# Optimization experiments

Measured on AMD Instinct MI355X. Metric: run time of the kernel, lower is better.

## Reference

```python
import jax, jax.numpy as jnp
import numpy as np

EMBED_DIM = 256
NUM_HEADS = 8
HEAD_DIM = EMBED_DIM // NUM_HEADS
SCALE = HEAD_DIM ** (-0.5)
L, B = 2048, 2


def setup_inputs() -> dict:
    key = jax.random.key(0)
    ks = jax.random.split(key, 12)
    s = EMBED_DIM ** (-0.5)
    return {
        "query": jax.random.normal(ks[0], (L, B, EMBED_DIM), jnp.float32),
        "key_": jax.random.normal(ks[1], (L, B, EMBED_DIM), jnp.float32),
        "value": jax.random.normal(ks[2], (L, B, EMBED_DIM), jnp.float32),
        "Wq": jax.random.normal(ks[3], (EMBED_DIM, EMBED_DIM), jnp.float32) * s,
        "bq": jnp.zeros((EMBED_DIM,), jnp.float32),
        "Wk": jax.random.normal(ks[4], (EMBED_DIM, EMBED_DIM), jnp.float32) * s,
        "bk": jnp.zeros((EMBED_DIM,), jnp.float32),
        "Wv": jax.random.normal(ks[5], (EMBED_DIM, EMBED_DIM), jnp.float32) * s,
        "bv": jnp.zeros((EMBED_DIM,), jnp.float32),
        "Wp": jax.random.normal(ks[6], (EMBED_DIM, EMBED_DIM), jnp.float32) * s,
        "bp": jnp.zeros((EMBED_DIM,), jnp.float32),
    }


def reference(query, key_, value, Wq, bq, Wk, bk, Wv, bv, Wp, bp):
    # Inputs are seq-first: [L, B, E]. Dropout treated as eval (identity).
    Lq, Bq, E = query.shape
    q = (query @ Wq + bq).reshape(Lq, Bq, NUM_HEADS, HEAD_DIM)
    k = (key_ @ Wk + bk).reshape(key_.shape[0], Bq, NUM_HEADS, HEAD_DIM)
    v = (value @ Wv + bv).reshape(value.shape[0], Bq, NUM_HEADS, HEAD_DIM)
    # scores: [B, H, Lq, Lk]
    attn = jnp.einsum('qbhd,kbhd->bhqk', q, k) * SCALE
    attn = jax.nn.softmax(attn, axis=-1)
    out = jnp.einsum('bhqk,kbhd->qbhd', attn, v).reshape(Lq, Bq, E)
    return out @ Wp + bp
```

## Files before the change

kernel.cpp:

```cpp
#include <hip/hip_runtime.h>
#include <math.h>

#define L_SEQ 2048
#define BATCH 2
#define EMB   256
#define NH    8
#define HD    32
#define NROW  (L_SEQ * BATCH)
#define SCALE 0.17677669529663687f
#define LOG2E 1.4426950408889634f

typedef __attribute__((ext_vector_type(8))) short          short8;
typedef __attribute__((ext_vector_type(8))) unsigned short ushort8v;
typedef __attribute__((ext_vector_type(4))) unsigned short ushort4v;
typedef __attribute__((ext_vector_type(4))) float          floatx4;

__device__ __forceinline__ unsigned short f2b(float x) {
    unsigned int u = __float_as_uint(x);
    unsigned int r = u + 0x7FFFu + ((u >> 16) & 1u);
    return (unsigned short)(r >> 16);
}

__device__ __forceinline__ unsigned int pack2bf(float lo, float hi) {
    unsigned int ulo = __float_as_uint(lo);
    unsigned int uhi = __float_as_uint(hi);
    ulo += 0x7FFFu + ((ulo >> 16) & 1u);
    uhi += 0x7FFFu + ((uhi >> 16) & 1u);
    return __builtin_amdgcn_perm(uhi, ulo, 0x07060302);
}

__device__ __forceinline__ float b2f(unsigned short u) {
    return __uint_as_float(((unsigned int)u) << 16);
}

__device__ __forceinline__ float hw_exp2(float x) {
    return __builtin_amdgcn_exp2f(x);
}

__global__ __launch_bounds__(256) void wtrans_kernel(const float* __restrict__ Wq,
                                                     const float* __restrict__ Wk,
                                                     const float* __restrict__ Wv,
                                                     const float* __restrict__ Wp,
                                                     unsigned short* __restrict__ out) {
    __shared__ unsigned short T[64][65];
    const int wsel = blockIdx.z;
    const float* W = (wsel == 0) ? Wq : (wsel == 1) ? Wk : (wsel == 2) ? Wv : Wp;
    const float scale = (wsel == 0) ? (SCALE * LOG2E) : 1.0f;
    unsigned short* dst = out + (size_t)wsel * EMB * EMB;
    const int k0 = blockIdx.x * 64, n0 = blockIdx.y * 64;
    const int tid = threadIdx.x;

    #pragma unroll
    for (int i = 0; i < 4; ++i) {
        int idx = tid + 256 * i;
        int r = idx >> 4, c4 = (idx & 15) * 4;
        float4 f = *(const float4*)&W[(size_t)(k0 + r) * EMB + n0 + c4];
        T[r][c4 + 0] = f2b(f.x * scale);
        T[r][c4 + 1] = f2b(f.y * scale);
        T[r][c4 + 2] = f2b(f.z * scale);
        T[r][c4 + 3] = f2b(f.w * scale);
    }
    __syncthreads();
    #pragma unroll
    for (int i = 0; i < 4; ++i) {
        int idx = tid + 256 * i;
        int rn = idx >> 4, ck = (idx & 15) * 4;
        ushort4v p;
        #pragma unroll
        for (int j = 0; j < 4; ++j) p[j] = T[ck + j][rn];
        *(ushort4v*)&dst[(size_t)(n0 + rn) * EMB + k0 + ck] = p;
    }
}

__global__ __launch_bounds__(256) void qkv_proj(const float* __restrict__ Xq,
                                                const float* __restrict__ Xk,
                                                const float* __restrict__ Xv,
                                                const unsigned short* __restrict__ Wt,
                                                const float* __restrict__ bq,
                                                const float* __restrict__ bk,
                                                const float* __restrict__ bv,
                                                unsigned short* __restrict__ outq,
                                                unsigned short* __restrict__ outk,
                                                unsigned short* __restrict__ outvt) {
    __shared__ unsigned short Xs[64][136];
    __shared__ unsigned short Ws[64][136];
    const int z = blockIdx.z;
    const float* X    = (z == 0) ? Xq : (z == 1) ? Xk : Xv;
    const float* bias = (z == 0) ? bq : (z == 1) ? bk : bv;
    const float bscale = (z == 0) ? (SCALE * LOG2E) : 1.0f;
    const unsigned short* W = Wt + (size_t)z * EMB * EMB;

    const int row0 = blockIdx.x * 64;
    const int col0 = blockIdx.y * 64;
    const int tid  = threadIdx.x;
    const int w    = tid >> 6;
    const int lane = tid & 63;
    const int l16  = lane & 15;
    const int quad = lane >> 4;
    const floatx4 zero4 = {0.f, 0.f, 0.f, 0.f};

    floatx4 acc[4] = {zero4, zero4, zero4, zero4};

    #pragma unroll
    for (int kh = 0; kh < 2; ++kh) {
        if (kh) __syncthreads();
        #pragma unroll
        for (int i = 0; i < 4; ++i) {
            int idx = tid + 256 * i;
            int r = idx >> 4, c8 = (idx & 15) * 8;
            const float4* xp = (const float4*)&X[(size_t)(row0 + r) * EMB + kh * 128 + c8];
            float4 f0 = xp[0], f1 = xp[1];
            uint4 pk;
            pk.x = pack2bf(f0.x, f0.y); pk.y = pack2bf(f0.z, f0.w);
            pk.z = pack2bf(f1.x, f1.y); pk.w = pack2bf(f1.z, f1.w);
            *(uint4*)&Xs[r][c8] = pk;
            *(ushort8v*)&Ws[r][c8] =
                *(const ushort8v*)&W[(size_t)(col0 + r) * EMB + kh * 128 + c8];
        }
        __syncthreads();

        #pragma unroll
        for (int k = 0; k < 128; k += 32) {
            short8 a = *(const short8*)&Xs[w * 16 + l16][k + quad * 8];
            #pragma unroll
            for (int g = 0; g < 4; ++g) {
                short8 bf = *(const short8*)&Ws[g * 16 + l16][k + quad * 8];
                acc[g] = __builtin_amdgcn_mfma_f32_16x16x32_bf16(a, bf, acc[g], 0, 0, 0);
            }
        }
    }

    if (z == 2) {
        __syncthreads();
        #pragma unroll
        for (int g = 0; g < 4; ++g) {
            int n = g * 16 + l16;
            float bb = bias[col0 + n] * bscale;
            #pragma unroll
            for (int r = 0; r < 4; ++r)
                Xs[w * 16 + quad * 4 + r][n] = f2b(acc[g][r] + bb);
        }
        __syncthreads();
        #pragma unroll
        for (int i = 0; i < 2; ++i) {
            int idx = tid + 256 * i;
            int n = idx >> 3, sub = idx & 7;
            int bb2 = sub >> 2, lq = sub & 3;
            ushort8v p;
            #pragma unroll
            for (int j = 0; j < 8; ++j) p[j] = Xs[(lq * 8 + j) * 2 + bb2][n];
            int h = (col0 + n) >> 5, d = (col0 + n) & 31;
            size_t base = ((size_t)(bb2 * NH + h) * HD + d) * L_SEQ + (row0 >> 1) + lq * 8;
            *(ushort8v*)&outvt[base] = p;
        }
    } else {
        unsigned short* outp = z ? outk : outq;
        #pragma unroll
        for (int g = 0; g < 4; ++g) {
            int c = col0 + g * 16 + l16;
            float bb = bias[c] * bscale;
            #pragma unroll
            for (int r = 0; r < 4; ++r) {
                int rg = row0 + w * 16 + quad * 4 + r;
                int b = rg & 1, ll = rg >> 1;
                int h = c >> 5, d = c & 31;
                outp[(((size_t)(b * NH + h) * L_SEQ) + ll) * HD + d] = f2b(acc[g][r] + bb);
            }
        }
    }
}

__global__ __launch_bounds__(256) void attn_kernel(const unsigned short* __restrict__ Q,
                                                   const unsigned short* __restrict__ K,
                                                   const unsigned short* __restrict__ Vt,
                                                   unsigned short* __restrict__ Opart,
                                                   float* __restrict__ lpart) {
    __shared__ unsigned short Vs[2][32][136];
    __shared__ unsigned short Ps[4][16][136];

    const int tid  = threadIdx.x;
    const int w    = tid >> 6;
    const int lane = tid & 63;
    const int l16  = lane & 15;
    const int quad = lane >> 4;

    const int l0   = blockIdx.x * 64;
    const int h    = blockIdx.y;
    const int b    = blockIdx.z & 1;
    const int half = blockIdx.z >> 1;
    const int koff = half * (L_SEQ / 2);
    const size_t bh = (size_t)(b * NH + h);

    const unsigned short* Qg  = Q  + (bh * L_SEQ) * HD;
    const unsigned short* Kg  = K  + (bh * L_SEQ + koff) * HD;
    const unsigned short* Vtg = Vt + (bh * HD) * L_SEQ + koff;

    short8 qfrag = *(const short8*)&Qg[(size_t)(l0 + w * 16 + l16) * HD + quad * 8];

    float lacc = 0.0f;
    const floatx4 zero4 = {0.f, 0.f, 0.f, 0.f};
    floatx4 o0 = zero4, o1 = zero4;

    const int vd = tid >> 3;
    const int vj = (tid & 7) * 8;

    short8 kf[8];
    #pragma unroll
    for (int g = 0; g < 8; ++g)
        kf[g] = *(const short8*)&Kg[(size_t)(g * 16 + l16) * HD + quad * 8];

    *(ushort8v*)&Vs[0][vd][vj]      = *(const ushort8v*)&Vtg[(size_t)vd * L_SEQ + vj];
    *(ushort8v*)&Vs[0][vd][64 + vj] = *(const ushort8v*)&Vtg[(size_t)vd * L_SEQ + 64 + vj];

    const int NT = (L_SEQ / 2) / 128;
    for (int kt = 0; kt < NT; ++kt) {
        __syncthreads();

        floatx4 s[8];
        #pragma unroll
        for (int g = 0; g < 8; ++g)
            s[g] = __builtin_amdgcn_mfma_f32_16x16x32_bf16(kf[g], qfrag, zero4, 0, 0, 0);

        ushort8v vn0, vn1;
        if (kt + 1 < NT) {
            #pragma unroll
            for (int g = 0; g < 8; ++g)
                kf[g] = *(const short8*)
                    &Kg[(size_t)((kt + 1) * 128 + g * 16 + l16) * HD + quad * 8];
            vn0 = *(const ushort8v*)&Vtg[(size_t)vd * L_SEQ + (kt + 1) * 128 + vj];
            vn1 = *(const ushort8v*)&Vtg[(size_t)vd * L_SEQ + (kt + 1) * 128 + 64 + vj];
        }

        #pragma unroll
        for (int g = 0; g < 8; ++g) {
            float p0 = hw_exp2(s[g][0]);
            float p1 = hw_exp2(s[g][1]);
            float p2 = hw_exp2(s[g][2]);
            float p3 = hw_exp2(s[g][3]);
            lacc += (p0 + p1) + (p2 + p3);
            uint2 pk;
            pk.x = pack2bf(p0, p1);
            pk.y = pack2bf(p2, p3);
            *(uint2*)&Ps[w][l16][g * 16 + quad * 4] = pk;
        }

        const unsigned short (*Vc)[136] = Vs[kt & 1];
        #pragma unroll
        for (int c = 0; c < 4; ++c) {
            short8 pf = *(const short8*)&Ps[w][l16][c * 32 + quad * 8];
            short8 va = *(const short8*)&Vc[l16][c * 32 + quad * 8];
            short8 vb = *(const short8*)&Vc[16 + l16][c * 32 + quad * 8];
            o0 = __builtin_amdgcn_mfma_f32_16x16x32_bf16(va, pf, o0, 0, 0, 0);
            o1 = __builtin_amdgcn_mfma_f32_16x16x32_bf16(vb, pf, o1, 0, 0, 0);
        }

        if (kt + 1 < NT) {
            *(ushort8v*)&Vs[(kt + 1) & 1][vd][vj]      = vn0;
            *(ushort8v*)&Vs[(kt + 1) & 1][vd][64 + vj] = vn1;
        }
    }

    lacc += __shfl_xor(lacc, 16);
    lacc += __shfl_xor(lacc, 32);

    int query = l0 + w * 16 + l16;
    if (lane < 16)
        lpart[(size_t)half * (BATCH * NH * L_SEQ) + bh * L_SEQ + query] = lacc;

    size_t base = (size_t)half * ((size_t)NROW * EMB) +
                  ((size_t)query * BATCH + b) * EMB + h * HD;
    uint2 e0, e1;
    e0.x = pack2bf(o0[0], o0[1]);
    e0.y = pack2bf(o0[2], o0[3]);
    e1.x = pack2bf(o1[0], o1[1]);
    e1.y = pack2bf(o1[2], o1[3]);
    *(uint2*)&Opart[base + quad * 4] = e0;
    *(uint2*)&Opart[base + 16 + quad * 4] = e1;
}

__global__ __launch_bounds__(256) void out_proj(const unsigned short* __restrict__ Opart,
                                                const float* __restrict__ lpart,
                                                const unsigned short* __restrict__ Wt,
                                                const float* __restrict__ bias,
                                                float* __restrict__ out) {
    __shared__ unsigned short Xs[32][264];
    __shared__ unsigned short Ws[32][264];
    const int row0 = blockIdx.x * 32;
    const int col0 = blockIdx.y * 32;
    const int tid  = threadIdx.x;
    const int w    = tid >> 6;
    const int rw   = (w & 1) * 16;
    const int cw   = (w >> 1) * 16;
    const int lane = tid & 63;
    const int l16  = lane & 15;
    const int quad = lane >> 4;

    const size_t OP = (size_t)NROW * EMB;
    const size_t LP = (size_t)BATCH * NH * L_SEQ;

    #pragma unroll
    for (int i = 0; i < 4; ++i) {
        int idx = tid + 256 * i;
        int r = idx >> 5, c8 = (idx & 31) * 8;
        int rg = row0 + r;
        int bb = rg & 1, q = rg >> 1, hh = c8 >> 5;
        size_t lidx = ((size_t)(bb * NH + hh)) * L_SEQ + q;
        float inv = __builtin_amdgcn_rcpf(lpart[lidx] + lpart[LP + lidx]);

        ushort8v u0 = *(const ushort8v*)&Opart[(size_t)rg * EMB + c8];
        ushort8v u1 = *(const ushort8v*)&Opart[OP + (size_t)rg * EMB + c8];
        uint4 pk;
        pk.x = pack2bf((b2f(u0[0]) + b2f(u1[0])) * inv, (b2f(u0[1]) + b2f(u1[1])) * inv);
        pk.y = pack2bf((b2f(u0[2]) + b2f(u1[2])) * inv, (b2f(u0[3]) + b2f(u1[3])) * inv);
        pk.z = pack2bf((b2f(u0[4]) + b2f(u1[4])) * inv, (b2f(u0[5]) + b2f(u1[5])) * inv);
        pk.w = pack2bf((b2f(u0[6]) + b2f(u1[6])) * inv, (b2f(u0[7]) + b2f(u1[7])) * inv);
        *(uint4*)&Xs[r][c8] = pk;

        *(ushort8v*)&Ws[r][c8] = *(const ushort8v*)&Wt[(size_t)(col0 + r) * EMB + c8];
    }
    __syncthreads();

    floatx4 acc = {0.f, 0.f, 0.f, 0.f};
    #pragma unroll
    for (int k = 0; k < EMB; k += 32) {
        short8 a  = *(const short8*)&Xs[rw + l16][k + quad * 8];
        short8 bf = *(const short8*)&Ws[cw + l16][k + quad * 8];
        acc = __builtin_amdgcn_mfma_f32_16x16x32_bf16(a, bf, acc, 0, 0, 0);
    }

    int c = col0 + cw + l16;
    float bb = bias[c];
    #pragma unroll
    for (int r = 0; r < 4; ++r) {
        int rg = row0 + rw + quad * 4 + r;
        out[(size_t)rg * EMB + c] = acc[r] + bb;
    }
}

extern "C" void kernel_launch(void* const* d_in, const int* in_sizes, int n_in,
                              void* d_out, int out_size, void* d_ws, size_t ws_size,
                              hipStream_t stream) {
    const float* query = (const float*)d_in[0];
    const float* key_  = (const float*)d_in[1];
    const float* value = (const float*)d_in[2];
    const float* Wq    = (const float*)d_in[3];
    const float* bq    = (const float*)d_in[4];
    const float* Wk    = (const float*)d_in[5];
    const float* bk    = (const float*)d_in[6];
    const float* Wv    = (const float*)d_in[7];
    const float* bv    = (const float*)d_in[8];
    const float* Wp    = (const float*)d_in[9];
    const float* bp    = (const float*)d_in[10];
    float* out = (float*)d_out;

    unsigned short* ws = (unsigned short*)d_ws;
    const size_t WSZ = (size_t)EMB * EMB;
    const size_t M   = (size_t)NROW * EMB;
    unsigned short* wt    = ws;
    unsigned short* qw    = ws + 4 * WSZ;
    unsigned short* kw    = qw + M;
    unsigned short* vtw   = kw + M;
    unsigned short* opart = vtw + M;
    float*          lpart = (float*)(opart + 2 * M);

    wtrans_kernel<<<dim3(4, 4, 4), 256, 0, stream>>>(Wq, Wk, Wv, Wp, wt);

    qkv_proj<<<dim3(NROW / 64, EMB / 64, 3), 256, 0, stream>>>(
        query, key_, value, wt, bq, bk, bv, qw, kw, vtw);

    attn_kernel<<<dim3(L_SEQ / 64, NH, BATCH * 2), 256, 0, stream>>>(
        qw, kw, vtw, opart, lpart);

    out_proj<<<dim3(NROW / 32, EMB / 32), 256, 0, stream>>>(
        opart, lpart, wt + 3 * WSZ, bp, out);
}
```

Before: 115.2 us.

## Keep softmax probabilities in registers via permlane16 swap instead of LDS round-trip

The attention kernel no longer writes exp'd scores to a per-wave shared-memory buffer and reads them back as an MFMA operand. It packs the probabilities to bf16, rearranges them across lane halves with v_permlane16_swap, and permutes the V-fragment column index so the K-dimension ordering matches. The Ps LDS buffer is removed and the barrier moves after the score MFMAs. The aim is to cut LDS traffic and latency in the inner loop. It depends on the permlane16_swap instruction being available on the target and on the permuted index mapping being correct.

```diff
diff --git a/kernel.cpp b/kernel.cpp
--- a/kernel.cpp
+++ b/kernel.cpp
@@ -14,6 +14,8 @@
 typedef __attribute__((ext_vector_type(8))) unsigned short ushort8v;
 typedef __attribute__((ext_vector_type(4))) unsigned short ushort4v;
 typedef __attribute__((ext_vector_type(4))) float          floatx4;
+typedef __attribute__((ext_vector_type(4))) unsigned int   uint4v;
+typedef __attribute__((ext_vector_type(2))) unsigned int   uint2v;
 
 __device__ __forceinline__ unsigned short f2b(float x) {
     unsigned int u = __float_as_uint(x);
@@ -21,7 +23,11 @@
     return (unsigned short)(r >> 16);
 }
 
-__device__ __forceinline__ unsigned int pack2bf(float lo, float hi) {
+__device__ __forceinline__ float b2f(unsigned short u) {
+    return __uint_as_float(((unsigned int)u) << 16);
+}
+
+__device__ __forceinline__ unsigned int pk_bf16(float lo, float hi) {
     unsigned int ulo = __float_as_uint(lo);
     unsigned int uhi = __float_as_uint(hi);
     ulo += 0x7FFFu + ((ulo >> 16) & 1u);
@@ -29,8 +35,13 @@
     return __builtin_amdgcn_perm(uhi, ulo, 0x07060302);
 }
 
-__device__ __forceinline__ float b2f(unsigned short u) {
-    return __uint_as_float(((unsigned int)u) << 16);
+__device__ __forceinline__ void pl16_swap(unsigned int& a, unsigned int& b) {
+#if __has_builtin(__builtin_amdgcn_permlane16_swap)
+    uint2v r = __builtin_amdgcn_permlane16_swap(a, b, false, false);
+    a = r[0]; b = r[1];
+#else
+    asm volatile("v_permlane16_swap_b32 %0, %1" : "+v"(a), "+v"(b));
+#endif
 }
 
 __device__ __forceinline__ float hw_exp2(float x) {
@@ -111,8 +122,8 @@
             const float4* xp = (const float4*)&X[(size_t)(row0 + r) * EMB + kh * 128 + c8];
             float4 f0 = xp[0], f1 = xp[1];
             uint4 pk;
-            pk.x = pack2bf(f0.x, f0.y); pk.y = pack2bf(f0.z, f0.w);
-            pk.z = pack2bf(f1.x, f1.y); pk.w = pack2bf(f1.z, f1.w);
+            pk.x = pk_bf16(f0.x, f0.y); pk.y = pk_bf16(f0.z, f0.w);
+            pk.z = pk_bf16(f1.x, f1.y); pk.w = pk_bf16(f1.z, f1.w);
             *(uint4*)&Xs[r][c8] = pk;
             *(ushort8v*)&Ws[r][c8] =
                 *(const ushort8v*)&W[(size_t)(col0 + r) * EMB + kh * 128 + c8];
@@ -176,13 +187,13 @@
                                                    unsigned short* __restrict__ Opart,
                                                    float* __restrict__ lpart) {
     __shared__ unsigned short Vs[2][32][136];
-    __shared__ unsigned short Ps[4][16][136];
 
     const int tid  = threadIdx.x;
     const int w    = tid >> 6;
     const int lane = tid & 63;
     const int l16  = lane & 15;
     const int quad = lane >> 4;
+    const int qs   = ((quad & 1) << 1) | (quad >> 1);
 
     const int l0   = blockIdx.x * 64;
     const int h    = blockIdx.y;
@@ -214,12 +225,12 @@
 
     const int NT = (L_SEQ / 2) / 128;
     for (int kt = 0; kt < NT; ++kt) {
-        __syncthreads();
-
         floatx4 s[8];
         #pragma unroll
         for (int g = 0; g < 8; ++g)
             s[g] = __builtin_amdgcn_mfma_f32_16x16x32_bf16(kf[g], qfrag, zero4, 0, 0, 0);
+
+        __syncthreads();
 
         ushort8v vn0, vn1;
         if (kt + 1 < NT) {
@@ -231,25 +242,24 @@
             vn1 = *(const ushort8v*)&Vtg[(size_t)vd * L_SEQ + (kt + 1) * 128 + 64 + vj];
         }
 
-        #pragma unroll
-        for (int g = 0; g < 8; ++g) {
-            float p0 = hw_exp2(s[g][0]);
-            float p1 = hw_exp2(s[g][1]);
-            float p2 = hw_exp2(s[g][2]);
-            float p3 = hw_exp2(s[g][3]);
-            lacc += (p0 + p1) + (p2 + p3);
-            uint2 pk;
-            pk.x = pack2bf(p0, p1);
-            pk.y = pack2bf(p2, p3);
-            *(uint2*)&Ps[w][l16][g * 16 + quad * 4] = pk;
-        }
-
         const unsigned short (*Vc)[136] = Vs[kt & 1];
         #pragma unroll
         for (int c = 0; c < 4; ++c) {
-            short8 pf = *(const short8*)&Ps[w][l16][c * 32 + quad * 8];
-            short8 va = *(const short8*)&Vc[l16][c * 32 + quad * 8];
-            short8 vb = *(const short8*)&Vc[16 + l16][c * 32 + quad * 8];
+            float a0 = hw_exp2(s[2 * c][0]),     a1 = hw_exp2(s[2 * c][1]);
+            float a2 = hw_exp2(s[2 * c][2]),     a3 = hw_exp2(s[2 * c][3]);
+            float b0 = hw_exp2(s[2 * c + 1][0]), b1 = hw_exp2(s[2 * c + 1][1]);
+            float b2 = hw_exp2(s[2 * c + 1][2]), b3 = hw_exp2(s[2 * c + 1][3]);
+            lacc += ((a0 + a1) + (a2 + a3)) + ((b0 + b1) + (b2 + b3));
+            unsigned int X  = pk_bf16(a0, a1);
+            unsigned int X2 = pk_bf16(a2, a3);
+            unsigned int Y  = pk_bf16(b0, b1);
+            unsigned int Y2 = pk_bf16(b2, b3);
+            pl16_swap(X, Y);
+            pl16_swap(X2, Y2);
+            uint4v pfu = {X, X2, Y, Y2};
+            short8 pf = __builtin_bit_cast(short8, pfu);
+            short8 va = *(const short8*)&Vc[l16][c * 32 + qs * 8];
+            short8 vb = *(const short8*)&Vc[16 + l16][c * 32 + qs * 8];
             o0 = __builtin_amdgcn_mfma_f32_16x16x32_bf16(va, pf, o0, 0, 0, 0);
             o1 = __builtin_amdgcn_mfma_f32_16x16x32_bf16(vb, pf, o1, 0, 0, 0);
         }
@@ -270,10 +280,10 @@
     size_t base = (size_t)half * ((size_t)NROW * EMB) +
                   ((size_t)query * BATCH + b) * EMB + h * HD;
     uint2 e0, e1;
-    e0.x = pack2bf(o0[0], o0[1]);
-    e0.y = pack2bf(o0[2], o0[3]);
-    e1.x = pack2bf(o1[0], o1[1]);
-    e1.y = pack2bf(o1[2], o1[3]);
+    e0.x = pk_bf16(o0[0], o0[1]);
+    e0.y = pk_bf16(o0[2], o0[3]);
+    e1.x = pk_bf16(o1[0], o1[1]);
+    e1.y = pk_bf16(o1[2], o1[3]);
     *(uint2*)&Opart[base + quad * 4] = e0;
     *(uint2*)&Opart[base + 16 + quad * 4] = e1;
 }
@@ -310,10 +320,10 @@
         ushort8v u0 = *(const ushort8v*)&Opart[(size_t)rg * EMB + c8];
         ushort8v u1 = *(const ushort8v*)&Opart[OP + (size_t)rg * EMB + c8];
         uint4 pk;
-        pk.x = pack2bf((b2f(u0[0]) + b2f(u1[0])) * inv, (b2f(u0[1]) + b2f(u1[1])) * inv);
-        pk.y = pack2bf((b2f(u0[2]) + b2f(u1[2])) * inv, (b2f(u0[3]) + b2f(u1[3])) * inv);
-        pk.z = pack2bf((b2f(u0[4]) + b2f(u1[4])) * inv, (b2f(u0[5]) + b2f(u1[5])) * inv);
-        pk.w = pack2bf((b2f(u0[6]) + b2f(u1[6])) * inv, (b2f(u0[7]) + b2f(u1[7])) * inv);
+        pk.x = pk_bf16((b2f(u0[0]) + b2f(u1[0])) * inv, (b2f(u0[1]) + b2f(u1[1])) * inv);
+        pk.y = pk_bf16((b2f(u0[2]) + b2f(u1[2])) * inv, (b2f(u0[3]) + b2f(u1[3])) * inv);
+        pk.z = pk_bf16((b2f(u0[4]) + b2f(u1[4])) * inv, (b2f(u0[5]) + b2f(u1[5])) * inv);
+        pk.w = pk_bf16((b2f(u0[6]) + b2f(u1[6])) * inv, (b2f(u0[7]) + b2f(u1[7])) * inv);
         *(uint4*)&Xs[r][c8] = pk;
 
         *(ushort8v*)&Ws[r][c8] = *(const ushort8v*)&Wt[(size_t)(col0 + r) * EMB + c8];
```

After: 115.1 us, median of 2. About the same (-0.1%).
